# Kernel tuning notes

Measured on AMD Instinct MI355X. Metric: run time of the kernel, lower is better.

Reference implementation:

```python
import jax, jax.numpy as jnp
import numpy as np

N = 50000
E = 800000
D_IN = 384
D_H = 128
D_MLP = 128
K = 16


def layer_norm(x, g, b, eps=1e-5):
    m = x.mean(-1, keepdims=True)
    v = ((x - m) ** 2).mean(-1, keepdims=True)
    return (x - m) / jnp.sqrt(v + eps) * g + b


def setup_inputs() -> dict:
    key = jax.random.key(0)
    ks = jax.random.split(key, 16)
    s = lambda d: 1.0 / np.sqrt(d)
    return {
        "x": jax.random.normal(ks[0], (N, D_IN), jnp.float32),
        "edge_index": jax.random.randint(ks[1], (2, E), 0, N, jnp.int64),
        # GCNConv 1
        "W1": jax.random.normal(ks[2], (D_IN, D_H), jnp.float32) * s(D_IN),
        "b1": jnp.zeros((D_H,), jnp.float32),
        "g1": jnp.ones((D_H,), jnp.float32),
        "be1": jnp.zeros((D_H,), jnp.float32),
        # GCNConv 2
        "W2": jax.random.normal(ks[3], (D_H, D_H), jnp.float32) * s(D_H),
        "b2": jnp.zeros((D_H,), jnp.float32),
        "g2": jnp.ones((D_H,), jnp.float32),
        "be2": jnp.zeros((D_H,), jnp.float32),
        # residual projection (input_dim != conv_hidden)
        "rW": jax.random.normal(ks[4], (D_IN, D_H), jnp.float32) * s(D_IN),
        "rb": jnp.zeros((D_H,), jnp.float32),
        "rg": jnp.ones((D_H,), jnp.float32),
        "rbe": jnp.zeros((D_H,), jnp.float32),
        # MLP head
        "mW1": jax.random.normal(ks[5], (D_H, D_MLP), jnp.float32) * s(D_H),
        "mb1": jnp.zeros((D_MLP,), jnp.float32),
        "mg": jnp.ones((D_MLP,), jnp.float32),
        "mbe": jnp.zeros((D_MLP,), jnp.float32),
        "mW2": jax.random.normal(ks[6], (D_MLP, K), jnp.float32) * s(D_MLP),
        "mb2": jnp.zeros((K,), jnp.float32),
    }


def reference(x, edge_index, W1, b1, g1, be1, W2, b2, g2, be2,
              rW, rb, rg, rbe, mW1, mb1, mg, mbe, mW2, mb2):
    n = x.shape[0]
    loops = jnp.arange(n, dtype=edge_index.dtype)
    src = jnp.concatenate([edge_index[0], loops])  # [E+N]
    dst = jnp.concatenate([edge_index[1], loops])
    # symmetric GCN normalization with self-loops
    deg = jax.ops.segment_sum(jnp.ones_like(src, x.dtype), dst, num_segments=n)
    dinv = jnp.where(deg > 0, jax.lax.rsqrt(deg), 0.0)
    norm = dinv[src] * dinv[dst]  # [E+N]

    def gcn_conv(h, W, b):
        hw = h @ W  # [N, D_H]
        msg = hw[src] * norm[:, None]  # gather + scale, [E+N, D_H]
        return jax.ops.segment_sum(msg, dst, num_segments=n) + b

    # layer 1 with projected residual
    h = jax.nn.elu(layer_norm(gcn_conv(x, W1, b1), g1, be1))
    h = h + layer_norm(x @ rW + rb, rg, rbe)
    # layer 2 with identity residual
    h = jax.nn.elu(layer_norm(gcn_conv(h, W2, b2), g2, be2)) + h
    # MLP head (dropout inactive in eval) + softmax over clusters
    z = jax.nn.elu(layer_norm(h @ mW1 + mb1, mg, mbe))
    H = z @ mW2 + mb2
    return jax.nn.softmax(H, axis=1)
```

## Files before the change

kernel.cpp:

```cpp
#include <hip/hip_runtime.h>

#define DH 128

typedef __attribute__((ext_vector_type(8))) short short8;
typedef __attribute__((ext_vector_type(4))) float f32x4;

__device__ __forceinline__ float wave_sum(float v) {
    #pragma unroll
    for (int o = 32; o > 0; o >>= 1) v += __shfl_xor(v, o, 64);
    return v;
}

__device__ __forceinline__ void ln_pair(float v0, float v1, float& o0, float& o1) {
    float m = wave_sum(v0 + v1) * (1.f / 128.f);
    float d0 = v0 - m, d1 = v1 - m;
    float var = wave_sum(d0 * d0 + d1 * d1) * (1.f / 128.f);
    float inv = rsqrtf(var + 1e-5f);
    o0 = d0 * inv; o1 = d1 * inv;
}

__device__ __forceinline__ float elu(float x) { return x > 0.f ? x : expm1f(x); }

__device__ __forceinline__ unsigned short f2bf(float f) {
    unsigned u = __float_as_uint(f);
    u += 0x7fffu + ((u >> 16) & 1u);
    return (unsigned short)(u >> 16);
}
__device__ __forceinline__ float bfl(unsigned u) { return __uint_as_float(u << 16); }
__device__ __forceinline__ float bfh(unsigned u) { return __uint_as_float(u & 0xffff0000u); }
__device__ __forceinline__ unsigned pack_bf2(float a, float b) {
    return (unsigned)f2bf(a) | ((unsigned)f2bf(b) << 16);
}
__device__ __forceinline__ short8 cvt8(float4 v0, float4 v1) {
    short8 o;
    o[0] = (short)f2bf(v0.x); o[1] = (short)f2bf(v0.y);
    o[2] = (short)f2bf(v0.z); o[3] = (short)f2bf(v0.w);
    o[4] = (short)f2bf(v1.x); o[5] = (short)f2bf(v1.y);
    o[6] = (short)f2bf(v1.z); o[7] = (short)f2bf(v1.w);
    return o;
}

__global__ void deg_count_k(const int* __restrict__ dst, int* __restrict__ deg, int E) {
    int e = blockIdx.x * 256 + threadIdx.x;
    if (e < E) atomicAdd(&deg[dst[e]], 1);
}

__global__ __launch_bounds__(1024) void scan_part_k(const int* __restrict__ deg,
                                                    int* __restrict__ rowptr,
                                                    int* __restrict__ bsum,
                                                    float* __restrict__ dinv, int n)
{
    __shared__ int wsum[16];
    const int tid = threadIdx.x, lane = tid & 63, wid = tid >> 6;
    int i = blockIdx.x * 1024 + tid;
    int v = (i < n) ? deg[i] : 0;
    if (i < n) dinv[i] = rsqrtf((float)(v + 1));
    int s = v;
    #pragma unroll
    for (int o = 1; o < 64; o <<= 1) {
        int t = __shfl_up(s, o, 64);
        if (lane >= o) s += t;
    }
    if (lane == 63) wsum[wid] = s;
    __syncthreads();
    if (tid < 16) {
        int ws = wsum[tid];
        #pragma unroll
        for (int o = 1; o < 16; o <<= 1) {
            int t = __shfl_up(ws, o, 64);
            if (tid >= o) ws += t;
        }
        wsum[tid] = ws;
    }
    __syncthreads();
    int excl = (wid ? wsum[wid - 1] : 0) + s - v;
    if (i < n) rowptr[i] = excl;
    if (tid == 0) bsum[blockIdx.x] = wsum[15];
}

__global__ void scan_top_k(int* __restrict__ bsum, int* __restrict__ rowptr_n, int nb) {
    int lane = threadIdx.x;
    int carry = 0;
    for (int base = 0; base < nb; base += 64) {
        int i = base + lane;
        int v = (i < nb) ? bsum[i] : 0;
        int s = v;
        #pragma unroll
        for (int o = 1; o < 64; o <<= 1) {
            int t = __shfl_up(s, o, 64);
            if (lane >= o) s += t;
        }
        if (i < nb) bsum[i] = carry + s - v;
        carry += __shfl(s, 63, 64);
    }
    if (lane == 0) *rowptr_n = carry;
}

__global__ void scan_add_k(const int* __restrict__ bsum, int* __restrict__ rowptr,
                           int* __restrict__ cursor, int n)
{
    int i = blockIdx.x * 256 + threadIdx.x;
    if (i < n) {
        int v = rowptr[i] + bsum[i >> 10];
        rowptr[i] = v;
        cursor[i] = v;
    }
}

__global__ void fill_k(const int* __restrict__ src, const int* __restrict__ dst,
                       const float* __restrict__ dinv, int* __restrict__ cursor,
                       int2* __restrict__ csr, int E)
{
    int e = blockIdx.x * 256 + threadIdx.x;
    if (e < E) {
        int s = src[e], d = dst[e];
        float w = dinv[s] * dinv[d];
        int p = atomicAdd(&cursor[d], 1);
        csr[p] = make_int2(s, __float_as_int(w));
    }
}

__global__ void repack_zero_k(const float* __restrict__ W1, const float* __restrict__ rW,
                              const float* __restrict__ W2, const float* __restrict__ mW1,
                              unsigned short* __restrict__ Wp, int* __restrict__ deg, int n)
{
    int idx = blockIdx.x * 256 + threadIdx.x;
    if (idx < n) deg[idx] = 0;
    if (idx >= 131072) return;
    const float* W; int base;
    if (idx < 49152)       { W = W1;  base = 0; }
    else if (idx < 98304)  { W = rW;  base = 49152; }
    else if (idx < 114688) { W = W2;  base = 98304; }
    else                   { W = mW1; base = 114688; }
    int l = idx - base;
    int kb = l >> 12, rem = l & 4095;
    int nn = rem >> 5, ki = rem & 31;
    Wp[idx] = f2bf(W[(kb * 32 + ki) * DH + nn]);
}

template<int K, int NV, bool AF32>
__global__ __launch_bounds__(256, 3) void mfma_gemm(
    const void* __restrict__ Avoid,
    const unsigned short* __restrict__ Bp1, const float* __restrict__ ba,
    const unsigned short* __restrict__ Bp2, const float* __restrict__ bb,
    unsigned short* __restrict__ outa, unsigned short* __restrict__ outb, int n)
{
    constexpr int NKB = K / 32;
    constexpr int SB   = NKB * 64 * 32;
    constexpr int SEP  = 128 * 72;
    constexpr int SMEM = SB > SEP ? SB : SEP;
    __shared__ __align__(16) unsigned short smem[SMEM];

    const int tid = threadIdx.x;
    const int wid = tid >> 6, lane = tid & 63;
    const int m16 = lane & 15, q = lane >> 4;

    const int nwg = gridDim.x;
    const int qc = nwg >> 3, rc = nwg & 7;
    const int xcd = blockIdx.x & 7, ix = blockIdx.x >> 3;
    const int work = (xcd < rc ? xcd * (qc + 1) : rc * (qc + 1) + (xcd - rc) * qc) + ix;
    const int rblk = work / NV;
    const int var  = work - rblk * NV;

    const int mat = (NV == 4) ? (var >> 1) : 0;
    const int c0  = (NV == 4) ? ((var & 1) * 64) : (var * 64);
    const unsigned short* Bp = mat ? Bp2 : Bp1;
    unsigned short* outp = mat ? outb : outa;
    const float* bias = mat ? bb : ba;
    const long long rowbase = (long long)rblk * 128;

    const unsigned short* A = (const unsigned short*)Avoid;
    const float* Af = (const float*)Avoid;

    long long r0 = rowbase + wid * 32 + m16;       if (r0 > (long long)n - 1) r0 = n - 1;
    long long r1 = rowbase + wid * 32 + 16 + m16;  if (r1 > (long long)n - 1) r1 = n - 1;

    f32x4 acc[2][4];
    const f32x4 zero = {0.f, 0.f, 0.f, 0.f};
    #pragma unroll
    for (int mi = 0; mi < 2; ++mi)
        #pragma unroll
        for (int nj = 0; nj < 4; ++nj) acc[mi][nj] = zero;

    short8 ha[3][2];
    float4 fa[3][2][2];
    short8 bf[2][4];

    auto fetchA = [&](int kb, int buf) {
        if constexpr (AF32) {
            const float* a0 = Af + r0 * K + kb * 32 + q * 8;
            const float* a1 = Af + r1 * K + kb * 32 + q * 8;
            fa[buf][0][0] = *(const float4*)a0;
            fa[buf][0][1] = *(const float4*)(a0 + 4);
            fa[buf][1][0] = *(const float4*)a1;
            fa[buf][1][1] = *(const float4*)(a1 + 4);
        } else {
            ha[buf][0] = *(const short8*)(A + r0 * K + kb * 32 + q * 8);
            ha[buf][1] = *(const short8*)(A + r1 * K + kb * 32 + q * 8);
        }
    };
    auto fetchB = [&](int kb, int buf) {
        #pragma unroll
        for (int nj = 0; nj < 4; ++nj)
            bf[buf][nj] = *(const short8*)(smem + kb * 2048 + (nj * 16 + m16) * 32 + q * 8);
    };

    fetchA(0, 0);
    if constexpr (NKB > 1) fetchA(1, 1);

    #pragma unroll
    for (int t = tid; t < K * 8; t += 256) {
        int k8 = t & 3, cl = (t >> 2) & 63, kb = t >> 8;
        *(short8*)(smem + kb * 2048 + cl * 32 + k8 * 8) =
            *(const short8*)(Bp + (long long)kb * 4096 + (c0 + cl) * 32 + k8 * 8);
    }
    __syncthreads();

    fetchB(0, 0);
    #pragma unroll
    for (int kb = 0; kb < NKB; ++kb) {
        if (kb + 2 < NKB) fetchA(kb + 2, (kb + 2) % 3);
        if (kb + 1 < NKB) fetchB(kb + 1, (kb + 1) & 1);
        const int ca = kb % 3, cb = kb & 1;
        short8 af[2];
        if constexpr (AF32) {
            af[0] = cvt8(fa[ca][0][0], fa[ca][0][1]);
            af[1] = cvt8(fa[ca][1][0], fa[ca][1][1]);
        } else {
            af[0] = ha[ca][0];
            af[1] = ha[ca][1];
        }
        #pragma unroll
        for (int mi = 0; mi < 2; ++mi)
            #pragma unroll
            for (int nj = 0; nj < 4; ++nj)
                acc[mi][nj] = __builtin_amdgcn_mfma_f32_16x16x32_bf16(af[mi], bf[cb][nj], acc[mi][nj], 0, 0, 0);
    }

    __syncthreads();
    #pragma unroll
    for (int nj = 0; nj < 4; ++nj) {
        int cl = nj * 16 + m16;
        float bv = bias ? bias[c0 + cl] : 0.f;
        #pragma unroll
        for (int mi = 0; mi < 2; ++mi)
            #pragma unroll
            for (int r = 0; r < 4; ++r)
                smem[(wid * 32 + mi * 16 + q * 4 + r) * 72 + cl] = f2bf(acc[mi][nj][r] + bv);
    }
    __syncthreads();
    #pragma unroll
    for (int h = 0; h < 4; ++h) {
        int idx = tid + h * 256;
        int row = idx >> 3, c8 = idx & 7;
        long long grow = rowbase + row;
        if (grow < n)
            *(short8*)(outp + grow * DH + c0 + c8 * 8) = *(const short8*)(smem + row * 72 + c8 * 8);
    }
}

__device__ __forceinline__ void gather_row(
    const unsigned* __restrict__ hw, const int2* __restrict__ csr,
    int beg, int end, int lane, float& o0, float& o1)
{
    float a0 = 0.f, a1 = 0.f, b0 = 0.f, b1 = 0.f;
    float c0 = 0.f, c1 = 0.f, d0 = 0.f, d1 = 0.f;
    int p = beg;
    for (; p + 7 < end; p += 8) {
        int2 e0 = csr[p],     e1 = csr[p + 1], e2 = csr[p + 2], e3 = csr[p + 3];
        int2 e4 = csr[p + 4], e5 = csr[p + 5], e6 = csr[p + 6], e7 = csr[p + 7];
        unsigned u0 = hw[(long long)e0.x * 64 + lane];
        unsigned u1 = hw[(long long)e1.x * 64 + lane];
        unsigned u2 = hw[(long long)e2.x * 64 + lane];
        unsigned u3 = hw[(long long)e3.x * 64 + lane];
        unsigned u4 = hw[(long long)e4.x * 64 + lane];
        unsigned u5 = hw[(long long)e5.x * 64 + lane];
        unsigned u6 = hw[(long long)e6.x * 64 + lane];
        unsigned u7 = hw[(long long)e7.x * 64 + lane];
        float w0 = __int_as_float(e0.y), w1 = __int_as_float(e1.y);
        float w2 = __int_as_float(e2.y), w3 = __int_as_float(e3.y);
        float w4 = __int_as_float(e4.y), w5 = __int_as_float(e5.y);
        float w6 = __int_as_float(e6.y), w7 = __int_as_float(e7.y);
        a0 = fmaf(w0, bfl(u0), a0);  a1 = fmaf(w0, bfh(u0), a1);
        b0 = fmaf(w1, bfl(u1), b0);  b1 = fmaf(w1, bfh(u1), b1);
        c0 = fmaf(w2, bfl(u2), c0);  c1 = fmaf(w2, bfh(u2), c1);
        d0 = fmaf(w3, bfl(u3), d0);  d1 = fmaf(w3, bfh(u3), d1);
        a0 = fmaf(w4, bfl(u4), a0);  a1 = fmaf(w4, bfh(u4), a1);
        b0 = fmaf(w5, bfl(u5), b0);  b1 = fmaf(w5, bfh(u5), b1);
        c0 = fmaf(w6, bfl(u6), c0);  c1 = fmaf(w6, bfh(u6), c1);
        d0 = fmaf(w7, bfl(u7), d0);  d1 = fmaf(w7, bfh(u7), d1);
    }
    for (; p + 3 < end; p += 4) {
        int2 e0 = csr[p], e1 = csr[p + 1], e2 = csr[p + 2], e3 = csr[p + 3];
        unsigned u0 = hw[(long long)e0.x * 64 + lane];
        unsigned u1 = hw[(long long)e1.x * 64 + lane];
        unsigned u2 = hw[(long long)e2.x * 64 + lane];
        unsigned u3 = hw[(long long)e3.x * 64 + lane];
        float w0 = __int_as_float(e0.y), w1 = __int_as_float(e1.y);
        float w2 = __int_as_float(e2.y), w3 = __int_as_float(e3.y);
        a0 = fmaf(w0, bfl(u0), a0);  a1 = fmaf(w0, bfh(u0), a1);
        b0 = fmaf(w1, bfl(u1), b0);  b1 = fmaf(w1, bfh(u1), b1);
        c0 = fmaf(w2, bfl(u2), c0);  c1 = fmaf(w2, bfh(u2), c1);
        d0 = fmaf(w3, bfl(u3), d0);  d1 = fmaf(w3, bfh(u3), d1);
    }
    for (; p < end; ++p) {
        int2 e0 = csr[p];
        unsigned u0 = hw[(long long)e0.x * 64 + lane];
        float w0 = __int_as_float(e0.y);
        a0 = fmaf(w0, bfl(u0), a0);
        a1 = fmaf(w0, bfh(u0), a1);
    }
    o0 = (a0 + b0) + (c0 + d0);
    o1 = (a1 + b1) + (c1 + d1);
}

__global__ __launch_bounds__(256) void gfuse1_k(
    const unsigned* __restrict__ hw, const unsigned* __restrict__ proj,
    const int* __restrict__ rowptr, const int2* __restrict__ csr,
    const float* __restrict__ dinv,
    const float* __restrict__ b1, const float* __restrict__ g1, const float* __restrict__ be1,
    const float* __restrict__ rg, const float* __restrict__ rbe,
    unsigned* __restrict__ hout, int n)
{
    int row = blockIdx.x * 4 + (threadIdx.x >> 6);
    if (row >= n) return;
    int lane = threadIdx.x & 63;
    float a0, a1;
    gather_row(hw, csr, rowptr[row], rowptr[row + 1], lane, a0, a1);
    long long off = (long long)row * 64;
    float di = dinv[row], sl = di * di;
    unsigned us = hw[off + lane];
    float2 bv  = *(const float2*)(b1 + 2 * lane);
    float2 gv  = *(const float2*)(g1 + 2 * lane);
    float2 bev = *(const float2*)(be1 + 2 * lane);
    float2 rgv = *(const float2*)(rg + 2 * lane);
    float2 rbv = *(const float2*)(rbe + 2 * lane);
    float v0 = a0 + sl * bfl(us) + bv.x;
    float v1 = a1 + sl * bfh(us) + bv.y;
    float o0, o1; ln_pair(v0, v1, o0, o1);
    float t0 = elu(o0 * gv.x + bev.x);
    float t1 = elu(o1 * gv.y + bev.y);
    unsigned up = proj[off + lane];
    float q0, q1; ln_pair(bfl(up), bfh(up), q0, q1);
    hout[off + lane] = pack_bf2(t0 + q0 * rgv.x + rbv.x, t1 + q1 * rgv.y + rbv.y);
}

__global__ __launch_bounds__(256) void gfuse2_k(
    const unsigned* __restrict__ hw, const unsigned* __restrict__ hprev,
    const int* __restrict__ rowptr, const int2* __restrict__ csr,
    const float* __restrict__ dinv,
    const float* __restrict__ b2, const float* __restrict__ g2, const float* __restrict__ be2,
    unsigned* __restrict__ h2, int n)
{
    int row = blockIdx.x * 4 + (threadIdx.x >> 6);
    if (row >= n) return;
    int lane = threadIdx.x & 63;
    float a0, a1;
    gather_row(hw, csr, rowptr[row], rowptr[row + 1], lane, a0, a1);
    long long off = (long long)row * 64;
    float di = dinv[row], sl = di * di;
    unsigned us = hw[off + lane];
    float2 bv  = *(const float2*)(b2 + 2 * lane);
    float2 gv  = *(const float2*)(g2 + 2 * lane);
    float2 bev = *(const float2*)(be2 + 2 * lane);
    float v0 = a0 + sl * bfl(us) + bv.x;
    float v1 = a1 + sl * bfh(us) + bv.y;
    float o0, o1; ln_pair(v0, v1, o0, o1);
    float t0 = elu(o0 * gv.x + bev.x);
    float t1 = elu(o1 * gv.y + bev.y);
    unsigned uh = hprev[off + lane];
    h2[off + lane] = pack_bf2(t0 + bfl(uh), t1 + bfh(uh));
}

__global__ __launch_bounds__(256) void head_k(
    const unsigned* __restrict__ zraw, const float* __restrict__ g, const float* __restrict__ be,
    const float* __restrict__ mW2, const float* __restrict__ mb2,
    float* __restrict__ out, int n)
{
    int row = blockIdx.x * 4 + (threadIdx.x >> 6);
    if (row >= n) return;
    int lane = threadIdx.x & 63;
    unsigned u = zraw[(long long)row * 64 + lane];
    float o0, o1; ln_pair(bfl(u), bfh(u), o0, o1);
    float2 gv  = *(const float2*)(g + 2 * lane);
    float2 bev = *(const float2*)(be + 2 * lane);
    float z0 = elu(o0 * gv.x + bev.x);
    float z1 = elu(o1 * gv.y + bev.y);
    int k = lane & 15, seg = lane >> 4;
    float acc = 0.f;
    #pragma unroll
    for (int t = 0; t < 16; ++t) {
        int srcl = seg * 16 + t;
        float zz0 = __shfl(z0, srcl, 64);
        float zz1 = __shfl(z1, srcl, 64);
        int c = seg * 32 + 2 * t;
        acc = fmaf(zz0, mW2[c * 16 + k], acc);
        acc = fmaf(zz1, mW2[(c + 1) * 16 + k], acc);
    }
    acc += __shfl_xor(acc, 32, 64);
    acc += __shfl_xor(acc, 16, 64);
    float hk = acc + mb2[k];
    float mx = hk;
    #pragma unroll
    for (int o = 8; o > 0; o >>= 1) mx = fmaxf(mx, __shfl_xor(mx, o, 64));
    float e = expf(hk - mx);
    float s = e;
    #pragma unroll
    for (int o = 8; o > 0; o >>= 1) s += __shfl_xor(s, o, 64);
    if (lane < 16) out[(long long)row * 16 + k] = e / s;
}

static inline size_t align16(size_t x) { return (x + 15) & ~(size_t)15; }

extern "C" void kernel_launch(void* const* d_in, const int* in_sizes, int n_in,
                              void* d_out, int out_size, void* d_ws, size_t ws_size,
                              hipStream_t stream)
{
    const float* x   = (const float*)d_in[0];
    const int*   ei  = (const int*)d_in[1];
    const float* W1  = (const float*)d_in[2];
    const float* b1  = (const float*)d_in[3];
    const float* g1  = (const float*)d_in[4];
    const float* be1 = (const float*)d_in[5];
    const float* W2  = (const float*)d_in[6];
    const float* b2  = (const float*)d_in[7];
    const float* g2  = (const float*)d_in[8];
    const float* be2 = (const float*)d_in[9];
    const float* rW  = (const float*)d_in[10];
    const float* rb  = (const float*)d_in[11];
    const float* rg  = (const float*)d_in[12];
    const float* rbe = (const float*)d_in[13];
    const float* mW1 = (const float*)d_in[14];
    const float* mb1 = (const float*)d_in[15];
    const float* mg  = (const float*)d_in[16];
    const float* mbe = (const float*)d_in[17];
    const float* mW2 = (const float*)d_in[18];
    const float* mb2 = (const float*)d_in[19];
    float* out = (float*)d_out;

    const int n = in_sizes[0] / 384;
    const int E = in_sizes[1] / 2;
    const int* src = ei;
    const int* dst = ei + E;

    char* w = (char*)d_ws;
    int* deg     = (int*)w;   w += align16((size_t)n * 4);
    int* rowptr  = (int*)w;   w += align16((size_t)(n + 1) * 4);
    int* cursor  = (int*)w;   w += align16((size_t)n * 4);
    float* dinv  = (float*)w; w += align16((size_t)n * 4);
    int* bsum    = (int*)w;   w += align16((size_t)1024 * 4);
    int2* csr    = (int2*)w;  w += align16((size_t)E * 8);
    unsigned short* hw1  = (unsigned short*)w; w += align16((size_t)n * DH * 2);
    unsigned short* proj = (unsigned short*)w; w += align16((size_t)n * DH * 2);
    unsigned short* hbuf = (unsigned short*)w; w += align16((size_t)n * DH * 2);
    unsigned short* Wp   = (unsigned short*)w; w += align16((size_t)131072 * 2);
    unsigned short* Wp1 = Wp;
    unsigned short* Wpr = Wp + 49152;
    unsigned short* Wp2 = Wp + 98304;
    unsigned short* WpM = Wp + 114688;
    unsigned short* hw2  = hw1;
    unsigned short* h2   = proj;
    unsigned short* zraw = hbuf;

    int gE = (E + 255) / 256;
    int gN = (n + 255) / 256;
    int nb = (n + 1023) / 1024;
    int rblks = (n + 127) / 128;
    int gRow4 = (n + 3) / 4;

    repack_zero_k<<<512, 256, 0, stream>>>(W1, rW, W2, mW1, Wp, deg, n);

    deg_count_k<<<gE, 256, 0, stream>>>(dst, deg, E);
    scan_part_k<<<nb, 1024, 0, stream>>>(deg, rowptr, bsum, dinv, n);
    scan_top_k<<<1, 64, 0, stream>>>(bsum, rowptr + n, nb);
    scan_add_k<<<gN, 256, 0, stream>>>(bsum, rowptr, cursor, n);
    fill_k<<<gE, 256, 0, stream>>>(src, dst, dinv, cursor, csr, E);

    mfma_gemm<384, 4, true><<<rblks * 4, 256, 0, stream>>>(x, Wp1, nullptr, Wpr, rb, hw1, proj, n);
    gfuse1_k<<<gRow4, 256, 0, stream>>>((unsigned*)hw1, (unsigned*)proj, rowptr, csr, dinv,
                                        b1, g1, be1, rg, rbe, (unsigned*)hbuf, n);

    mfma_gemm<128, 2, false><<<rblks * 2, 256, 0, stream>>>(hbuf, Wp2, nullptr, nullptr, nullptr, hw2, nullptr, n);
    gfuse2_k<<<gRow4, 256, 0, stream>>>((unsigned*)hw2, (unsigned*)hbuf, rowptr, csr, dinv,
                                        b2, g2, be2, (unsigned*)h2, n);

    mfma_gemm<128, 2, false><<<rblks * 2, 256, 0, stream>>>(h2, WpM, mb1, nullptr, nullptr, zraw, nullptr, n);
    head_k<<<gRow4, 256, 0, stream>>>((unsigned*)zraw, mg, mbe, mW2, mb2, out, n);
}
```

Baseline: 418.5 us.

## Stream A and B tiles through double-buffered LDS in MFMA GEMM

Restructures the MFMA GEMM so that both A and B k-tiles are staged cooperatively through a fixed-size double-buffered shared-memory area. Previously each wave fetched A directly into registers with a triple buffer, and the whole B panel was preloaded into LDS. Shared memory and register use are now smaller and fixed, which allows raising launch bounds to 4 blocks per CU for higher occupancy. The cost is a barrier on every k-step and an extra round trip through LDS for A.

```diff
diff --git a/kernel.cpp b/kernel.cpp
--- a/kernel.cpp
+++ b/kernel.cpp
@@ -139,17 +139,14 @@
 }
 
 template<int K, int NV, bool AF32>
-__global__ __launch_bounds__(256, 3) void mfma_gemm(
+__global__ __launch_bounds__(256, 4) void mfma_gemm(
     const void* __restrict__ Avoid,
     const unsigned short* __restrict__ Bp1, const float* __restrict__ ba,
     const unsigned short* __restrict__ Bp2, const float* __restrict__ bb,
     unsigned short* __restrict__ outa, unsigned short* __restrict__ outb, int n)
 {
     constexpr int NKB = K / 32;
-    constexpr int SB   = NKB * 64 * 32;
-    constexpr int SEP  = 128 * 72;
-    constexpr int SMEM = SB > SEP ? SB : SEP;
-    __shared__ __align__(16) unsigned short smem[SMEM];
+    __shared__ __align__(16) unsigned short smem[12288];
 
     const int tid = threadIdx.x;
     const int wid = tid >> 6, lane = tid & 63;
@@ -169,11 +166,53 @@
     const float* bias = mat ? bb : ba;
     const long long rowbase = (long long)rblk * 128;
 
-    const unsigned short* A = (const unsigned short*)Avoid;
+    unsigned short* smA = smem;
+    unsigned short* smB = smem + 8192;
+
+    const int aq0 = tid >> 7,        ar0 = tid & 127;
+    const int aq1 = (tid + 256) >> 7, ar1 = tid & 127;
+    long long gr0 = rowbase + ar0; if (gr0 > (long long)n - 1) gr0 = n - 1;
+    long long gr1 = rowbase + ar1; if (gr1 > (long long)n - 1) gr1 = n - 1;
+    const int qb = tid >> 6, clb = tid & 63;
+
     const float* Af = (const float*)Avoid;
-
-    long long r0 = rowbase + wid * 32 + m16;       if (r0 > (long long)n - 1) r0 = n - 1;
-    long long r1 = rowbase + wid * 32 + 16 + m16;  if (r1 > (long long)n - 1) r1 = n - 1;
+    const unsigned short* Ah = (const unsigned short*)Avoid;
+    const float* pAf0 = AF32 ? Af + gr0 * K + aq0 * 8 : nullptr;
+    const float* pAf1 = AF32 ? Af + gr1 * K + aq1 * 8 : nullptr;
+    const unsigned short* pAh0 = AF32 ? nullptr : Ah + gr0 * K + aq0 * 8;
+    const unsigned short* pAh1 = AF32 ? nullptr : Ah + gr1 * K + aq1 * 8;
+    const unsigned short* pB = Bp + (c0 + clb) * 32 + qb * 8;
+
+    unsigned short* dA0 = smA + aq0 * 1024 + ar0 * 8;
+    unsigned short* dA1 = smA + aq1 * 1024 + ar1 * 8;
+    unsigned short* dB  = smB + qb * 512 + clb * 8;
+
+    float4 raf[2][2][2];
+    short8 rah[2][2];
+    short8 rbv[2];
+
+    auto loadT = [&](int kb, int buf) {
+        if constexpr (AF32) {
+            raf[buf][0][0] = *(const float4*)(pAf0 + kb * 32);
+            raf[buf][0][1] = *(const float4*)(pAf0 + kb * 32 + 4);
+            raf[buf][1][0] = *(const float4*)(pAf1 + kb * 32);
+            raf[buf][1][1] = *(const float4*)(pAf1 + kb * 32 + 4);
+        } else {
+            rah[buf][0] = *(const short8*)(pAh0 + kb * 32);
+            rah[buf][1] = *(const short8*)(pAh1 + kb * 32);
+        }
+        rbv[buf] = *(const short8*)(pB + kb * 4096);
+    };
+    auto writeT = [&](int buf) {
+        if constexpr (AF32) {
+            *(short8*)(dA0 + buf * 4096) = cvt8(raf[buf][0][0], raf[buf][0][1]);
+            *(short8*)(dA1 + buf * 4096) = cvt8(raf[buf][1][0], raf[buf][1][1]);
+        } else {
+            *(short8*)(dA0 + buf * 4096) = rah[buf][0];
+            *(short8*)(dA1 + buf * 4096) = rah[buf][1];
+        }
+        *(short8*)(dB + buf * 2048) = rbv[buf];
+    };
 
     f32x4 acc[2][4];
     const f32x4 zero = {0.f, 0.f, 0.f, 0.f};
@@ -182,62 +221,33 @@
         #pragma unroll
         for (int nj = 0; nj < 4; ++nj) acc[mi][nj] = zero;
 
-    short8 ha[3][2];
-    float4 fa[3][2][2];
-    short8 bf[2][4];
-
-    auto fetchA = [&](int kb, int buf) {
-        if constexpr (AF32) {
-            const float* a0 = Af + r0 * K + kb * 32 + q * 8;
-            const float* a1 = Af + r1 * K + kb * 32 + q * 8;
-            fa[buf][0][0] = *(const float4*)a0;
-            fa[buf][0][1] = *(const float4*)(a0 + 4);
-            fa[buf][1][0] = *(const float4*)a1;
-            fa[buf][1][1] = *(const float4*)(a1 + 4);
-        } else {
-            ha[buf][0] = *(const short8*)(A + r0 * K + kb * 32 + q * 8);
-            ha[buf][1] = *(const short8*)(A + r1 * K + kb * 32 + q * 8);
+    const unsigned short* fa_base = smA + q * 1024 + (wid * 32 + m16) * 8;
+    const unsigned short* fb_base = smB + q * 512 + m16 * 8;
+
+    loadT(0, 0);
+    if constexpr (NKB > 1) loadT(1, 1);
+    writeT(0);
+    __syncthreads();
+
+    #pragma unroll
+    for (int kb = 0; kb < NKB; ++kb) {
+        const int buf = kb & 1;
+        short8 af0 = *(const short8*)(fa_base + buf * 4096);
+        short8 af1 = *(const short8*)(fa_base + buf * 4096 + 128);
+        short8 bf[4];
+        #pragma unroll
+        for (int nj = 0; nj < 4; ++nj)
+            bf[nj] = *(const short8*)(fb_base + buf * 2048 + nj * 128);
+        if (kb + 2 < NKB) loadT(kb + 2, kb & 1);
+        if (kb + 1 < NKB) writeT((kb + 1) & 1);
+        #pragma unroll
+        for (int nj = 0; nj < 4; ++nj) {
+            acc[0][nj] = __builtin_amdgcn_mfma_f32_16x16x32_bf16(af0, bf[nj], acc[0][nj], 0, 0, 0);
+            acc[1][nj] = __builtin_amdgcn_mfma_f32_16x16x32_bf16(af1, bf[nj], acc[1][nj], 0, 0, 0);
         }
-    };
-    auto fetchB = [&](int kb, int buf) {
-        #pragma unroll
-        for (int nj = 0; nj < 4; ++nj)
-            bf[buf][nj] = *(const short8*)(smem + kb * 2048 + (nj * 16 + m16) * 32 + q * 8);
-    };
-
-    fetchA(0, 0);
-    if constexpr (NKB > 1) fetchA(1, 1);
-
-    #pragma unroll
-    for (int t = tid; t < K * 8; t += 256) {
-        int k8 = t & 3, cl = (t >> 2) & 63, kb = t >> 8;
-        *(short8*)(smem + kb * 2048 + cl * 32 + k8 * 8) =
-            *(const short8*)(Bp + (long long)kb * 4096 + (c0 + cl) * 32 + k8 * 8);
-    }
-    __syncthreads();
-
-    fetchB(0, 0);
-    #pragma unroll
-    for (int kb = 0; kb < NKB; ++kb) {
-        if (kb + 2 < NKB) fetchA(kb + 2, (kb + 2) % 3);
-        if (kb + 1 < NKB) fetchB(kb + 1, (kb + 1) & 1);
-        const int ca = kb % 3, cb = kb & 1;
-        short8 af[2];
-        if constexpr (AF32) {
-            af[0] = cvt8(fa[ca][0][0], fa[ca][0][1]);
-            af[1] = cvt8(fa[ca][1][0], fa[ca][1][1]);
-        } else {
-            af[0] = ha[ca][0];
-            af[1] = ha[ca][1];
-        }
-        #pragma unroll
-        for (int mi = 0; mi < 2; ++mi)
-            #pragma unroll
-            for (int nj = 0; nj < 4; ++nj)
-                acc[mi][nj] = __builtin_amdgcn_mfma_f32_16x16x32_bf16(af[mi], bf[cb][nj], acc[mi][nj], 0, 0, 0);
-    }
-
-    __syncthreads();
+        __syncthreads();
+    }
+
     #pragma unroll
     for (int nj = 0; nj < 4; ++nj) {
         int cl = nj * 16 + m16;
```

Measured after the change: 430.9 us. +2.9%, slower.
